# Kernel tuning notes

Measured on AMD Instinct MI355X. Metric: run time of the kernel, lower is better.

Reference implementation:

```python
import jax, jax.numpy as jnp
import numpy as np

IGNORE_LABEL = 255
THRESH = 0.9
MIN_KEPT = 10000


def setup_inputs() -> dict:
    key = jax.random.key(0)
    k1, k2 = jax.random.split(key)
    n, c, d, h, w = 2, 12, 64, 128, 128
    predict = jax.random.normal(k1, (n, c, d, h, w), dtype=jnp.float32)
    target = jax.random.randint(k2, (n, d, h, w), 0, c, dtype=jnp.int64)
    return {"predict": predict, "target": target}


def reference(predict, target):
    n, c, d, h, w = predict.shape
    # rollaxis(predict, 1).reshape(c, -1): class-major flattening, matching target.ravel()
    logits = jnp.moveaxis(predict, 1, 0).reshape(c, -1)          # (c, N)
    labels = target.reshape(-1)                                   # (N,)
    valid = labels != IGNORE_LABEL
    safe_lab = jnp.where(valid, labels, 0)

    logp = jax.nn.log_softmax(logits, axis=0)                     # (c, N), stable softmax
    lp_at_label = jnp.take_along_axis(logp, safe_lab[None, :], axis=0)[0]  # (N,)
    prob_at_label = jnp.exp(lp_at_label)                          # softmax prob of true class

    num_valid = valid.sum()
    # k-th smallest true-class prob among valid pixels (invalid -> +inf pushed to end)
    sorted_prob = jnp.sort(jnp.where(valid, prob_at_label, jnp.inf))
    k_idx = jnp.maximum(jnp.minimum(MIN_KEPT, num_valid) - 1, 0)
    th_val = sorted_prob[k_idx]
    threshold = jnp.maximum(th_val, THRESH)

    # if min_kept >= num_valid: keep all valid; else keep hard examples (prob <= threshold)
    keep_all = MIN_KEPT >= num_valid
    kept = valid & jnp.where(keep_all, True, prob_at_label <= threshold)

    # masked mean cross-entropy (CrossEntropyLoss with ignore_index, mean reduction)
    nll = -lp_at_label
    num = jnp.sum(jnp.where(kept, nll, 0.0))
    cnt = jnp.sum(kept)
    loss = num / jnp.maximum(cnt, 1).astype(nll.dtype)
    return loss
```

## Files before the change

kernel.cpp:

```cpp
#include <hip/hip_runtime.h>
#include <hip/hip_bf16.h>
#include <math.h>


#define IGNORE_LABEL 255
#define MIN_KEPT 10000u

constexpr int   C         = 12;
constexpr int   PIX_SHIFT = 20;
constexpr int   PIX_MASK  = (1 << PIX_SHIFT) - 1;
constexpr int   NBINS     = 2048;
constexpr float BIN_SCALE = (float)NBINS / 0.1f;

struct Ws {
    double       sum_p3;
    unsigned int cnt_p3;
    unsigned int flag;
    float        threshold;
    unsigned int done;
    unsigned int done2;
    unsigned int pad[9];
    unsigned int hist[NBINS];
};

__device__ inline float wave_reduce_f(float v) {
    #pragma unroll
    for (int o = 32; o > 0; o >>= 1) v += __shfl_down(v, o, 64);
    return v;
}
__device__ inline unsigned int wave_reduce_u(unsigned int v) {
    #pragma unroll
    for (int o = 32; o > 0; o >>= 1) v += __shfl_down(v, o, 64);
    return v;
}
__device__ inline double wave_reduce_d(double v) {
    #pragma unroll
    for (int o = 32; o > 0; o >>= 1) v += __shfl_down(v, o, 64);
    return v;
}

__device__ inline void stage16(const float* g, float* l) {
    __builtin_amdgcn_global_load_lds(
        (const __attribute__((address_space(1))) void*)g,
        (__attribute__((address_space(3))) void*)l,
        16, 0, 0);
}

__global__ __launch_bounds__(256, 3) void main_pass_kernel(
        const float* __restrict__ pred, const int* __restrict__ tgt,
        Ws* __restrict__ ws, uint4* __restrict__ partials, int npix) {
    __shared__ float smem[6 * 2048];

    const int blk   = blockIdx.x;
    const int t     = threadIdx.x;
    const int wave  = t >> 6, lane = t & 63;
    const int bpix0 = blk << 11;
    if (bpix0 >= npix) return;

    const size_t sbase = (((size_t)(bpix0 >> PIX_SHIFT) * C) << PIX_SHIFT)
                       + (size_t)(bpix0 & PIX_MASK);

    const int4 la = *(const int4*)(tgt + bpix0 + (t << 2));
    const int4 lb = *(const int4*)(tgt + bpix0 + 1024 + (t << 2));
    const int lab[8] = {la.x, la.y, la.z, la.w, lb.x, lb.y, lb.z, lb.w};

    float E[8]  = {0,0,0,0,0,0,0,0};
    float ll[8] = {0,0,0,0,0,0,0,0};

    const float* gw = pred + sbase + (wave << 9) + (lane << 2);

    #pragma unroll
    for (int ph = 0; ph < 2; ++ph) {
        #pragma unroll
        for (int ci = 0; ci < 6; ++ci) {
            const int c = ph * 6 + ci;
            const float* g0 = gw + ((size_t)c << PIX_SHIFT);
            float* l0 = smem + (ci << 11) + (wave << 9);
            stage16(g0,       l0);
            stage16(g0 + 256, l0 + 256);
        }
        __syncthreads();

        #pragma unroll
        for (int ci = 0; ci < 6; ++ci) {
            const int c = ph * 6 + ci;
            const float4 v0 = *(const float4*)(smem + (ci << 11) + (t << 2));
            const float4 v1 = *(const float4*)(smem + (ci << 11) + 1024 + (t << 2));
            const float vv[8] = {v0.x, v0.y, v0.z, v0.w, v1.x, v1.y, v1.z, v1.w};
            #pragma unroll
            for (int j = 0; j < 8; ++j) {
                E[j] += __expf(vv[j]);
                if (lab[j] == c) ll[j] = vv[j];
            }
        }
        __syncthreads();
    }

    float        my_sle = 0.0f, my_sva = 0.0f;
    unsigned int my_cle = 0u,   my_cva = 0u;
    #pragma unroll
    for (int j = 0; j < 8; ++j) {
        const float ls   = __logf(E[j]);
        const float nll  = ls - ll[j];
        const float prob = __expf(ll[j] - ls);
        if (lab[j] != IGNORE_LABEL) {
            my_cva += 1u;
            my_sva += nll;
            if (prob <= 0.9f) {
                my_cle += 1u;
                my_sle += nll;
            } else {
                int b = (int)((prob - 0.9f) * BIN_SCALE);
                b = b < 0 ? 0 : (b >= NBINS - 1 ? NBINS - 1 : b);
                atomicAdd(&ws->hist[b], 1u);
            }
        }
    }

    __shared__ float        s_le[4], s_va[4];
    __shared__ unsigned int s_cle[4], s_cva[4];
    const float        r_le = wave_reduce_f(my_sle);
    const float        r_va = wave_reduce_f(my_sva);
    const unsigned int r_cl = wave_reduce_u(my_cle);
    const unsigned int r_cv = wave_reduce_u(my_cva);
    if (lane == 0) { s_le[wave] = r_le; s_va[wave] = r_va; s_cle[wave] = r_cl; s_cva[wave] = r_cv; }
    __syncthreads();
    if (t == 0) {
        uint4 p;
        p.x = __float_as_uint(s_le[0] + s_le[1] + s_le[2] + s_le[3]);
        p.y = __float_as_uint(s_va[0] + s_va[1] + s_va[2] + s_va[3]);
        p.z = s_cle[0] + s_cle[1] + s_cle[2] + s_cle[3];
        p.w = s_cva[0] + s_cva[1] + s_cva[2] + s_cva[3];
        partials[blk] = p;
    }
}

__global__ __launch_bounds__(1024) void reduce_finalize_kernel(
        Ws* __restrict__ ws, const uint4* __restrict__ partials,
        int nblocks, float* __restrict__ out) {
    double       sle = 0.0, sva = 0.0;
    unsigned int cle = 0u,  cva = 0u;
    for (int i = threadIdx.x; i < nblocks; i += 1024) {
        const uint4 p = partials[i];
        sle += (double)__uint_as_float(p.x);
        sva += (double)__uint_as_float(p.y);
        cle += p.z;
        cva += p.w;
    }
    __shared__ double       d_le[16], d_va[16];
    __shared__ unsigned int u_le[16], u_va[16];
    const int wid = threadIdx.x >> 6, lane = threadIdx.x & 63;
    const double       r_sle = wave_reduce_d(sle);
    const double       r_sva = wave_reduce_d(sva);
    const unsigned int r_cle = wave_reduce_u(cle);
    const unsigned int r_cva = wave_reduce_u(cva);
    if (lane == 0) { d_le[wid] = r_sle; d_va[wid] = r_sva; u_le[wid] = r_cle; u_va[wid] = r_cva; }
    __syncthreads();
    if (threadIdx.x == 0) {
        double       t_sle = 0.0, t_sva = 0.0;
        unsigned int t_cle = 0u,  t_cva = 0u;
        #pragma unroll
        for (int i = 0; i < 16; ++i) {
            t_sle += d_le[i]; t_sva += d_va[i]; t_cle += u_le[i]; t_cva += u_va[i];
        }
        const unsigned int nv = t_cva;
        const unsigned int k  = nv < MIN_KEPT ? nv : MIN_KEPT;
        if (MIN_KEPT >= nv) {
            out[0] = (float)(t_sva / (double)(nv > 0u ? nv : 1u));
            ws->flag = 0u;
        } else if (t_cle >= k) {
            out[0] = (float)(t_sle / (double)(t_cle > 0u ? t_cle : 1u));
            ws->flag = 0u;
        } else {
            unsigned int cum = t_cle;
            int b = NBINS - 1;
            for (int i = 0; i < NBINS; ++i) {
                cum += ws->hist[i];
                if (cum >= k) { b = i; break; }
            }
            ws->threshold = 0.9f + (float)(b + 1) * (0.1f / (float)NBINS);
            ws->flag = 1u;
            out[0] = 0.0f;
        }
    }
}

__global__ __launch_bounds__(256) void fallback_kernel(
        const float* __restrict__ pred, const int* __restrict__ tgt,
        Ws* __restrict__ ws, float* __restrict__ out, int npix_q) {
    if (ws->flag == 0u) return;
    const float th = ws->threshold;
    const int stride = gridDim.x * blockDim.x;

    float        my_s = 0.0f;
    unsigned int my_c = 0u;
    for (int t = blockIdx.x * blockDim.x + threadIdx.x; t < npix_q; t += stride) {
        const int p0 = t << 2;
        const float* base = pred +
            (((size_t)(p0 >> PIX_SHIFT) * C) << PIX_SHIFT) + (p0 & PIX_MASK);
        const int4 li = *(const int4*)(tgt + p0);
        const int lab[4] = {li.x, li.y, li.z, li.w};
        float s[4] = {0,0,0,0}, l_lab[4] = {0,0,0,0};
        #pragma unroll
        for (int ci = 0; ci < C; ++ci) {
            const float4 v = *(const float4*)(base + ((size_t)ci << PIX_SHIFT));
            const float vv[4] = {v.x, v.y, v.z, v.w};
            #pragma unroll
            for (int j = 0; j < 4; ++j) {
                s[j] += __expf(vv[j]);
                if (lab[j] == ci) l_lab[j] = vv[j];
            }
        }
        #pragma unroll
        for (int j = 0; j < 4; ++j) {
            const float ls   = __logf(s[j]);
            const float nll  = ls - l_lab[j];
            const float prob = __expf(l_lab[j] - ls);
            if (lab[j] != IGNORE_LABEL && prob <= th) { my_c += 1u; my_s += nll; }
        }
    }
    __shared__ float        s_s[4];
    __shared__ unsigned int s_c[4];
    const int wid = threadIdx.x >> 6, lane = threadIdx.x & 63;
    const float        r_s = wave_reduce_f(my_s);
    const unsigned int r_c = wave_reduce_u(my_c);
    if (lane == 0) { s_s[wid] = r_s; s_c[wid] = r_c; }
    __syncthreads();
    if (threadIdx.x == 0) {
        const float        t_s = s_s[0] + s_s[1] + s_s[2] + s_s[3];
        const unsigned int t_c = s_c[0] + s_c[1] + s_c[2] + s_c[3];
        if (t_s != 0.0f) atomicAdd(&ws->sum_p3, (double)t_s);
        if (t_c)         atomicAdd(&ws->cnt_p3, t_c);
        __threadfence();
        const unsigned int prev = atomicAdd(&ws->done2, 1u);
        if (prev == gridDim.x - 1u) {
            const unsigned int cnt = ws->cnt_p3;
            out[0] = (float)(ws->sum_p3 / (double)(cnt > 0u ? cnt : 1u));
        }
    }
}

extern "C" void kernel_launch(void* const* d_in, const int* in_sizes, int n_in,
                              void* d_out, int out_size, void* d_ws, size_t ws_size,
                              hipStream_t stream) {
    const float* pred = (const float*)d_in[0];
    const int*   tgt  = (const int*)d_in[1];
    float*       out  = (float*)d_out;
    Ws*          ws   = (Ws*)d_ws;
    uint4*       partials = (uint4*)((char*)d_ws + sizeof(Ws));

    const int npix   = in_sizes[1];
    const int npix_q = npix >> 2;
    const int blocks = (npix + 2047) / 2048;

    hipMemsetAsync(d_ws, 0, sizeof(Ws), stream);
    main_pass_kernel<<<blocks, 256, 0, stream>>>(pred, tgt, ws, partials, npix);
    reduce_finalize_kernel<<<1, 1024, 0, stream>>>(ws, partials, blocks, out);
    fallback_kernel<<<128, 256, 0, stream>>>(pred, tgt, ws, out, npix_q);
}
```

Measured before the change: 161.8 us.

## Double-buffer class staging into LDS with explicit vmcnt waits

Replaces the two-phase load-then-compute loop over 6 classes with a four-phase double-buffered pipeline of 3 classes each. The next group's global-to-LDS loads are issued before the current group is computed. Manual s_waitcnt vmcnt/lgkmcnt plus raw s_barrier replace __syncthreads, so memory latency overlaps with the exp/accumulate work. LDS use per block stays the same. The hand-counted vmcnt values must match the number of outstanding loads, or the kernel reads stale data.

```diff
diff --git a/kernel.cpp b/kernel.cpp
--- a/kernel.cpp
+++ b/kernel.cpp
@@ -49,7 +49,7 @@
 __global__ __launch_bounds__(256, 3) void main_pass_kernel(
         const float* __restrict__ pred, const int* __restrict__ tgt,
         Ws* __restrict__ ws, uint4* __restrict__ partials, int npix) {
-    __shared__ float smem[6 * 2048];
+    __shared__ float smem[2 * 3 * 2048];
 
     const int blk   = blockIdx.x;
     const int t     = threadIdx.x;
@@ -69,32 +69,65 @@
 
     const float* gw = pred + sbase + (wave << 9) + (lane << 2);
 
-    #pragma unroll
-    for (int ph = 0; ph < 2; ++ph) {
-        #pragma unroll
-        for (int ci = 0; ci < 6; ++ci) {
-            const int c = ph * 6 + ci;
-            const float* g0 = gw + ((size_t)c << PIX_SHIFT);
-            float* l0 = smem + (ci << 11) + (wave << 9);
-            stage16(g0,       l0);
-            stage16(g0 + 256, l0 + 256);
-        }
-        __syncthreads();
-
-        #pragma unroll
-        for (int ci = 0; ci < 6; ++ci) {
-            const int c = ph * 6 + ci;
-            const float4 v0 = *(const float4*)(smem + (ci << 11) + (t << 2));
-            const float4 v1 = *(const float4*)(smem + (ci << 11) + 1024 + (t << 2));
-            const float vv[8] = {v0.x, v0.y, v0.z, v0.w, v1.x, v1.y, v1.z, v1.w};
-            #pragma unroll
-            for (int j = 0; j < 8; ++j) {
-                E[j] += __expf(vv[j]);
-                if (lab[j] == c) ll[j] = vv[j];
-            }
-        }
-        __syncthreads();
-    }
+#define STAGE(ph, buf) do {                                                  \
+        _Pragma("unroll")                                                    \
+        for (int ci = 0; ci < 3; ++ci) {                                     \
+            const int c_ = (ph) * 3 + ci;                                    \
+            const float* g0_ = gw + ((size_t)c_ << PIX_SHIFT);               \
+            float* l0_ = smem + (buf) * 6144 + ci * 2048 + (wave << 9);      \
+            stage16(g0_,       l0_);                                         \
+            stage16(g0_ + 256, l0_ + 256);                                   \
+        }                                                                    \
+        asm volatile("" ::: "memory");              \
+    } while (0)
+
+#define COMPUTE(ph, buf) do {                                                \
+        _Pragma("unroll")                                                    \
+        for (int ci = 0; ci < 3; ++ci) {                                     \
+            const int c_ = (ph) * 3 + ci;                                    \
+            const float4 v0_ = *(const float4*)(smem + (buf) * 6144 +        \
+                                                ci * 2048 + (t << 2));       \
+            const float4 v1_ = *(const float4*)(smem + (buf) * 6144 +        \
+                                                ci * 2048 + 1024 + (t << 2));\
+            const float vv_[8] = {v0_.x, v0_.y, v0_.z, v0_.w,                \
+                                  v1_.x, v1_.y, v1_.z, v1_.w};               \
+            _Pragma("unroll")                                                \
+            for (int j = 0; j < 8; ++j) {                                    \
+                E[j] += __expf(vv_[j]);                                      \
+                if (lab[j] == c_) ll[j] = vv_[j];                            \
+            }                                                                \
+        }                                                                    \
+    } while (0)
+
+#define WAITV6()  asm volatile("s_waitcnt vmcnt(6)"  ::: "memory")
+#define WAITV0()  asm volatile("s_waitcnt vmcnt(0)"  ::: "memory")
+#define WAITL0()  asm volatile("s_waitcnt lgkmcnt(0)" ::: "memory")
+
+    STAGE(0, 0);
+
+    STAGE(1, 1);
+    WAITV6();  __builtin_amdgcn_s_barrier();
+    COMPUTE(0, 0);
+    WAITL0();  __builtin_amdgcn_s_barrier();
+
+    STAGE(2, 0);
+    WAITV6();  __builtin_amdgcn_s_barrier();
+    COMPUTE(1, 1);
+    WAITL0();  __builtin_amdgcn_s_barrier();
+
+    STAGE(3, 1);
+    WAITV6();  __builtin_amdgcn_s_barrier();
+    COMPUTE(2, 0);
+    WAITL0();  __builtin_amdgcn_s_barrier();
+
+    WAITV0();  __builtin_amdgcn_s_barrier();
+    COMPUTE(3, 1);
+
+#undef STAGE
+#undef COMPUTE
+#undef WAITV6
+#undef WAITV0
+#undef WAITL0
 
     float        my_sle = 0.0f, my_sva = 0.0f;
     unsigned int my_cle = 0u,   my_cva = 0u;
```

After: 160.6 us. Within noise of the previous version (-0.7%).
